# Optimization experiments

Measured on AMD Instinct MI355X. Metric: run time of the kernel, lower is better.

Reference implementation:

```python
import jax, jax.numpy as jnp
import numpy as np

NEG = -1000.0  # fill value for unmatched (type_mask != ti) entries

B, N, R = 4, 48, 16
T = 2 * R + 1          # 33 transition channels
Nc, L = 80, 3          # chains, chain length
Nt, Ni = 16, 5         # triples, chains per triple (uniform c_sections)


def setup_inputs() -> dict:
    key = jax.random.key(0)
    k1, k2, k3, k4, k5 = jax.random.split(key, 5)
    transitions = jax.random.normal(k1, (B, N, N, T), dtype=jnp.float32)
    type_mask = jax.random.randint(k2, (B, N, N, R), 0, 2, dtype=jnp.int32)
    rules = jax.random.randint(k3, (Nc, L), 0, T, dtype=jnp.int32)
    # stacked per-triple weights [Nt, Ni] (orig: ParameterList of [Ni,1]) and biases [Nt]
    weights = jax.random.normal(k4, (Nt, Ni), dtype=jnp.float32) / np.sqrt(Ni)
    biases = jax.random.uniform(k5, (Nt,), dtype=jnp.float32, minval=-1.0, maxval=1.0)
    return {"transitions": transitions, "type_mask": type_mask, "rules": rules,
            "weights": weights, "biases": biases}


def path_scores(transitions, rules):
    """Tropical (max-plus) chain DP.
    transitions: [B,N,N,T], rules: [Nc,L] -> scores [B,N,N,Nc]
    scores[b,x,y,c] = max over intermediate nodes of sum of hop scores.
    """
    Lc = rules.shape[1]
    hops = [transitions[..., rules[:, l]] for l in range(Lc)]  # each [B,N,N,Nc]
    # max-plus "matmul": s[b,x,y,c] = max_k hops0[b,x,k,c] + hops1[b,k,y,c]
    s = jnp.max(hops[0][:, :, :, None, :] + hops[1][:, None, :, :, :], axis=2)
    for l in range(2, Lc):
        s = jnp.max(s[:, :, :, None, :] + hops[l][:, None, :, :, :], axis=2)
    return s


def reference(transitions, type_mask, rules, weights, biases):
    # scores over all chains, exponentiated: [B,N,N,Nc]
    s = jnp.exp(path_scores(transitions, rules))
    # group chains by triple (uniform sections): [B,N,N,Nt,Ni]
    s = s.reshape(s.shape[0], s.shape[1], s.shape[2], Nt, Ni)
    # per-triple weighted sum + bias; one triple per relation so Nt == R
    comb = jnp.einsum('bxytc,tc->bxyt', s, weights) + biases  # [B,N,N,R]
    # masked_scatter: write score where type_mask[...,i] == ti (== 0 here), else -1000
    out = jnp.where(type_mask == 0, comb, NEG)
    return out
```

## Files before the change

kernel.cpp:

```cpp
#include <hip/hip_runtime.h>
#include <cmath>

#define BB 4
#define NN 48
#define PP (NN * NN)
#define TT 33
#define RR 16
#define NC 80
#define NI 5
#define NEG (-1000.0f)

#define XS 24
#define XP 25

__global__ __launch_bounds__(256) void transpose_kernel(
    const float* __restrict__ trans,
    float*       __restrict__ tpose)
{
    __shared__ float tile[64 * TT];
    const int blk = blockIdx.x;
    const int b   = blk / 36;
    const int p0  = (blk - b * 36) * 64;

    const float4* src = (const float4*)(trans + ((size_t)b * PP + p0) * TT);
    for (int j = threadIdx.x; j < 64 * TT / 4; j += 256)
        ((float4*)tile)[j] = src[j];
    __syncthreads();

    for (int j = threadIdx.x; j < TT * 64; j += 256) {
        const int t  = j >> 6;
        const int pl = j & 63;
        tpose[((size_t)b * TT + t) * PP + p0 + pl] = tile[pl * TT + t];
    }
}

__global__ __launch_bounds__(192) void chain_dp_kernel(
    const float* __restrict__ tpose,
    const int*   __restrict__ rules,
    const float* __restrict__ weights,
    float*       __restrict__ sw)
{
    __shared__ float H0T[NN * XP];
    __shared__ float H1 [PP];
    __shared__ float H2 [PP];
    __shared__ float S1T[NN * XP];

    const int blk = blockIdx.x;
    const int bc  = blk >> 1;
    const int xh  = blk & 1;
    const int b   = bc / NC;
    const int c   = bc - b * NC;
    const int xbase = xh * XS;

    const int r0 = rules[c * 3 + 0];
    const int r1 = rules[c * 3 + 1];
    const int r2 = rules[c * 3 + 2];

    const float* p0 = tpose + ((size_t)b * TT + r0) * PP + xbase * NN;
    const float* p1 = tpose + ((size_t)b * TT + r1) * PP;
    const float* p2 = tpose + ((size_t)b * TT + r2) * PP;

    for (int j = threadIdx.x; j < PP / 4; j += 192) {
        ((float4*)H1)[j] = ((const float4*)p1)[j];
        ((float4*)H2)[j] = ((const float4*)p2)[j];
    }
    for (int j = threadIdx.x; j < XS * NN / 4; j += 192) {
        const float4 v0 = ((const float4*)p0)[j];
        const int xl = (4 * j) / NN;
        const int k  = (4 * j) - xl * NN;
        H0T[(k + 0) * XP + xl] = v0.x;
        H0T[(k + 1) * XP + xl] = v0.y;
        H0T[(k + 2) * XP + xl] = v0.z;
        H0T[(k + 3) * XP + xl] = v0.w;
    }
    __syncthreads();

    const int tx = threadIdx.x & 7;
    const int ty = threadIdx.x >> 3;
    const int x0 = tx * 3;
    const int y0 = ty * 2;

    float acc[3][2];
    #pragma unroll
    for (int jx = 0; jx < 3; ++jx) {
        acc[jx][0] = -INFINITY; acc[jx][1] = -INFINITY;
    }

    #pragma unroll 4
    for (int kp = 0; kp < NN / 2; ++kp) {
        const int k = kp * 2;
        float a0[3], a1[3];
        #pragma unroll
        for (int jx = 0; jx < 3; ++jx) {
            a0[jx] = H0T[k * XP + x0 + jx];
            a1[jx] = H0T[(k + 1) * XP + x0 + jx];
        }
        const float2 bv0 = *(const float2*)&H1[k * NN + y0];
        const float2 bv1 = *(const float2*)&H1[(k + 1) * NN + y0];
        #pragma unroll
        for (int jx = 0; jx < 3; ++jx) {
            acc[jx][0] = fmaxf(acc[jx][0], fmaxf(a0[jx] + bv0.x, a1[jx] + bv1.x));
            acc[jx][1] = fmaxf(acc[jx][1], fmaxf(a0[jx] + bv0.y, a1[jx] + bv1.y));
        }
    }

    #pragma unroll
    for (int jx = 0; jx < 3; ++jx) {
        S1T[(y0 + 0) * XP + x0 + jx] = acc[jx][0];
        S1T[(y0 + 1) * XP + x0 + jx] = acc[jx][1];
    }
    __syncthreads();

    float acc2[3][2];
    #pragma unroll
    for (int jx = 0; jx < 3; ++jx) {
        acc2[jx][0] = -INFINITY; acc2[jx][1] = -INFINITY;
    }

    #pragma unroll 4
    for (int kp = 0; kp < NN / 2; ++kp) {
        const int k = kp * 2;
        float a0[3], a1[3];
        #pragma unroll
        for (int jx = 0; jx < 3; ++jx) {
            a0[jx] = S1T[k * XP + x0 + jx];
            a1[jx] = S1T[(k + 1) * XP + x0 + jx];
        }
        const float2 bv0 = *(const float2*)&H2[k * NN + y0];
        const float2 bv1 = *(const float2*)&H2[(k + 1) * NN + y0];
        #pragma unroll
        for (int jx = 0; jx < 3; ++jx) {
            acc2[jx][0] = fmaxf(acc2[jx][0], fmaxf(a0[jx] + bv0.x, a1[jx] + bv1.x));
            acc2[jx][1] = fmaxf(acc2[jx][1], fmaxf(a0[jx] + bv0.y, a1[jx] + bv1.y));
        }
    }

    const float wgt = weights[c];
    float* outp = sw + (size_t)bc * PP;
    #pragma unroll
    for (int jx = 0; jx < 3; ++jx) {
        float2 o;
        o.x = __expf(acc2[jx][0]) * wgt;
        o.y = __expf(acc2[jx][1]) * wgt;
        *(float2*)&outp[(xbase + x0 + jx) * NN + y0] = o;
    }
}

__global__ __launch_bounds__(256) void combine_kernel(
    const float* __restrict__ sw,
    const int*   __restrict__ mask,
    const float* __restrict__ biases,
    float*       __restrict__ out)
{
    const int quad = threadIdx.x >> 6;
    const int pl   = blockIdx.x * 64 + (threadIdx.x & 63);
    const int b = pl / PP;
    const int p = pl - b * PP;

    const float* base = sw + (size_t)b * NC * PP + p;

    float acc[4];
    #pragma unroll
    for (int tt = 0; tt < 4; ++tt) {
        const int t = quad * 4 + tt;
        float s = biases[t];
        #pragma unroll
        for (int i = 0; i < NI; ++i)
            s += base[(size_t)(t * NI + i) * PP];
        acc[tt] = s;
    }

    const int4 m = *(const int4*)(mask + (size_t)pl * RR + quad * 4);
    float4 o;
    o.x = (m.x == 0) ? acc[0] : NEG;
    o.y = (m.y == 0) ? acc[1] : NEG;
    o.z = (m.z == 0) ? acc[2] : NEG;
    o.w = (m.w == 0) ? acc[3] : NEG;
    *(float4*)(out + (size_t)pl * RR + quad * 4) = o;
}

extern "C" void kernel_launch(void* const* d_in, const int* in_sizes, int n_in,
                              void* d_out, int out_size, void* d_ws, size_t ws_size,
                              hipStream_t stream)
{
    const float* trans   = (const float*)d_in[0];
    const int*   mask    = (const int*)  d_in[1];
    const int*   rules   = (const int*)  d_in[2];
    const float* weights = (const float*)d_in[3];
    const float* biases  = (const float*)d_in[4];
    float* out = (float*)d_out;

    float* tpose = (float*)d_ws;
    float* sw    = tpose + (size_t)BB * TT * PP;

    transpose_kernel<<<BB * 36, 256, 0, stream>>>(trans, tpose);

    chain_dp_kernel<<<BB * NC * 2, 192, 0, stream>>>(tpose, rules, weights, sw);

    combine_kernel<<<BB * PP / 64, 256, 0, stream>>>(sw, mask, biases, out);
}
```

Before: 75.38 us.

## Fuse chain DP with per-triple combine and mask, dropping intermediate buffer

The chain DP kernel and the combine kernel are merged. Each block now handles one (batch, triple, x-half), loops over the triple's 5 chains, and accumulates the weighted exp scores in registers before applying bias and mask and writing the output directly. This removes the large intermediate sw buffer round trip and one launch. In exchange the grid shrinks from 640 to 128 blocks, each doing five sequential chain iterations with extra syncs, and the output and mask accesses are strided by 16 and uncoalesced.

```diff
diff --git a/kernel.cpp b/kernel.cpp
--- a/kernel.cpp
+++ b/kernel.cpp
@@ -12,6 +12,7 @@
 
 #define XS 24
 #define XP 25
+#define NTH 384
 
 __global__ __launch_bounds__(256) void transpose_kernel(
     const float* __restrict__ trans,
@@ -34,11 +35,13 @@
     }
 }
 
-__global__ __launch_bounds__(192) void chain_dp_kernel(
+__global__ __launch_bounds__(NTH) void fused_scorer(
     const float* __restrict__ tpose,
     const int*   __restrict__ rules,
     const float* __restrict__ weights,
-    float*       __restrict__ sw)
+    const float* __restrict__ biases,
+    const int*   __restrict__ mask,
+    float*       __restrict__ out)
 {
     __shared__ float H0T[NN * XP];
     __shared__ float H1 [PP];
@@ -46,137 +49,83 @@
     __shared__ float S1T[NN * XP];
 
     const int blk = blockIdx.x;
-    const int bc  = blk >> 1;
     const int xh  = blk & 1;
-    const int b   = bc / NC;
-    const int c   = bc - b * NC;
+    const int bt  = blk >> 1;
+    const int b   = bt >> 4;
+    const int t   = bt & 15;
     const int xbase = xh * XS;
 
-    const int r0 = rules[c * 3 + 0];
-    const int r1 = rules[c * 3 + 1];
-    const int r2 = rules[c * 3 + 2];
+    const int xl = threadIdx.x >> 4;
+    const int yt = threadIdx.x & 15;
+    const int y0 = yt * 3;
 
-    const float* p0 = tpose + ((size_t)b * TT + r0) * PP + xbase * NN;
-    const float* p1 = tpose + ((size_t)b * TT + r1) * PP;
-    const float* p2 = tpose + ((size_t)b * TT + r2) * PP;
+    float acc_out[3] = {0.0f, 0.0f, 0.0f};
 
-    for (int j = threadIdx.x; j < PP / 4; j += 192) {
-        ((float4*)H1)[j] = ((const float4*)p1)[j];
-        ((float4*)H2)[j] = ((const float4*)p2)[j];
-    }
-    for (int j = threadIdx.x; j < XS * NN / 4; j += 192) {
-        const float4 v0 = ((const float4*)p0)[j];
-        const int xl = (4 * j) / NN;
-        const int k  = (4 * j) - xl * NN;
-        H0T[(k + 0) * XP + xl] = v0.x;
-        H0T[(k + 1) * XP + xl] = v0.y;
-        H0T[(k + 2) * XP + xl] = v0.z;
-        H0T[(k + 3) * XP + xl] = v0.w;
-    }
-    __syncthreads();
+    for (int ci = 0; ci < NI; ++ci) {
+        const int c  = t * NI + ci;
+        const int r0 = rules[c * 3 + 0];
+        const int r1 = rules[c * 3 + 1];
+        const int r2 = rules[c * 3 + 2];
+        const float w = weights[c];
 
-    const int tx = threadIdx.x & 7;
-    const int ty = threadIdx.x >> 3;
-    const int x0 = tx * 3;
-    const int y0 = ty * 2;
+        const float* p0 = tpose + ((size_t)b * TT + r0) * PP + xbase * NN;
+        const float* p1 = tpose + ((size_t)b * TT + r1) * PP;
+        const float* p2 = tpose + ((size_t)b * TT + r2) * PP;
 
-    float acc[3][2];
-    #pragma unroll
-    for (int jx = 0; jx < 3; ++jx) {
-        acc[jx][0] = -INFINITY; acc[jx][1] = -INFINITY;
+        __syncthreads();
+
+        for (int j = threadIdx.x; j < PP / 4; j += NTH) {
+            ((float4*)H1)[j] = ((const float4*)p1)[j];
+            ((float4*)H2)[j] = ((const float4*)p2)[j];
+        }
+        for (int j = threadIdx.x; j < XS * NN / 4; j += NTH) {
+            const float4 v0 = ((const float4*)p0)[j];
+            const int x = (4 * j) / NN;
+            const int k = (4 * j) - x * NN;
+            H0T[(k + 0) * XP + x] = v0.x;
+            H0T[(k + 1) * XP + x] = v0.y;
+            H0T[(k + 2) * XP + x] = v0.z;
+            H0T[(k + 3) * XP + x] = v0.w;
+        }
+        __syncthreads();
+
+        float a0 = -INFINITY, a1 = -INFINITY, a2 = -INFINITY;
+        #pragma unroll 4
+        for (int kp = 0; kp < NN / 2; ++kp) {
+            const int k = kp * 2;
+            const float h0 = H0T[k * XP + xl];
+            const float h1 = H0T[(k + 1) * XP + xl];
+            a0 = fmaxf(a0, fmaxf(h0 + H1[k * NN + y0 + 0], h1 + H1[(k + 1) * NN + y0 + 0]));
+            a1 = fmaxf(a1, fmaxf(h0 + H1[k * NN + y0 + 1], h1 + H1[(k + 1) * NN + y0 + 1]));
+            a2 = fmaxf(a2, fmaxf(h0 + H1[k * NN + y0 + 2], h1 + H1[(k + 1) * NN + y0 + 2]));
+        }
+        S1T[(y0 + 0) * XP + xl] = a0;
+        S1T[(y0 + 1) * XP + xl] = a1;
+        S1T[(y0 + 2) * XP + xl] = a2;
+        __syncthreads();
+
+        float s0 = -INFINITY, s1 = -INFINITY, s2 = -INFINITY;
+        #pragma unroll 4
+        for (int kp = 0; kp < NN / 2; ++kp) {
+            const int k = kp * 2;
+            const float h0 = S1T[k * XP + xl];
+            const float h1 = S1T[(k + 1) * XP + xl];
+            s0 = fmaxf(s0, fmaxf(h0 + H2[k * NN + y0 + 0], h1 + H2[(k + 1) * NN + y0 + 0]));
+            s1 = fmaxf(s1, fmaxf(h0 + H2[k * NN + y0 + 1], h1 + H2[(k + 1) * NN + y0 + 1]));
+            s2 = fmaxf(s2, fmaxf(h0 + H2[k * NN + y0 + 2], h1 + H2[(k + 1) * NN + y0 + 2]));
+        }
+        acc_out[0] += w * __expf(s0);
+        acc_out[1] += w * __expf(s1);
+        acc_out[2] += w * __expf(s2);
     }
 
-    #pragma unroll 4
-    for (int kp = 0; kp < NN / 2; ++kp) {
-        const int k = kp * 2;
-        float a0[3], a1[3];
-        #pragma unroll
-        for (int jx = 0; jx < 3; ++jx) {
-            a0[jx] = H0T[k * XP + x0 + jx];
-            a1[jx] = H0T[(k + 1) * XP + x0 + jx];
-        }
-        const float2 bv0 = *(const float2*)&H1[k * NN + y0];
-        const float2 bv1 = *(const float2*)&H1[(k + 1) * NN + y0];
-        #pragma unroll
-        for (int jx = 0; jx < 3; ++jx) {
-            acc[jx][0] = fmaxf(acc[jx][0], fmaxf(a0[jx] + bv0.x, a1[jx] + bv1.x));
-            acc[jx][1] = fmaxf(acc[jx][1], fmaxf(a0[jx] + bv0.y, a1[jx] + bv1.y));
-        }
+    const float bias = biases[t];
+    const int xg = xbase + xl;
+    #pragma unroll
+    for (int j = 0; j < 3; ++j) {
+        const size_t oidx = ((size_t)(b * PP + xg * NN + y0 + j)) * RR + t;
+        out[oidx] = (mask[oidx] == 0) ? (acc_out[j] + bias) : NEG;
     }
-
-    #pragma unroll
-    for (int jx = 0; jx < 3; ++jx) {
-        S1T[(y0 + 0) * XP + x0 + jx] = acc[jx][0];
-        S1T[(y0 + 1) * XP + x0 + jx] = acc[jx][1];
-    }
-    __syncthreads();
-
-    float acc2[3][2];
-    #pragma unroll
-    for (int jx = 0; jx < 3; ++jx) {
-        acc2[jx][0] = -INFINITY; acc2[jx][1] = -INFINITY;
-    }
-
-    #pragma unroll 4
-    for (int kp = 0; kp < NN / 2; ++kp) {
-        const int k = kp * 2;
-        float a0[3], a1[3];
-        #pragma unroll
-        for (int jx = 0; jx < 3; ++jx) {
-            a0[jx] = S1T[k * XP + x0 + jx];
-            a1[jx] = S1T[(k + 1) * XP + x0 + jx];
-        }
-        const float2 bv0 = *(const float2*)&H2[k * NN + y0];
-        const float2 bv1 = *(const float2*)&H2[(k + 1) * NN + y0];
-        #pragma unroll
-        for (int jx = 0; jx < 3; ++jx) {
-            acc2[jx][0] = fmaxf(acc2[jx][0], fmaxf(a0[jx] + bv0.x, a1[jx] + bv1.x));
-            acc2[jx][1] = fmaxf(acc2[jx][1], fmaxf(a0[jx] + bv0.y, a1[jx] + bv1.y));
-        }
-    }
-
-    const float wgt = weights[c];
-    float* outp = sw + (size_t)bc * PP;
-    #pragma unroll
-    for (int jx = 0; jx < 3; ++jx) {
-        float2 o;
-        o.x = __expf(acc2[jx][0]) * wgt;
-        o.y = __expf(acc2[jx][1]) * wgt;
-        *(float2*)&outp[(xbase + x0 + jx) * NN + y0] = o;
-    }
-}
-
-__global__ __launch_bounds__(256) void combine_kernel(
-    const float* __restrict__ sw,
-    const int*   __restrict__ mask,
-    const float* __restrict__ biases,
-    float*       __restrict__ out)
-{
-    const int quad = threadIdx.x >> 6;
-    const int pl   = blockIdx.x * 64 + (threadIdx.x & 63);
-    const int b = pl / PP;
-    const int p = pl - b * PP;
-
-    const float* base = sw + (size_t)b * NC * PP + p;
-
-    float acc[4];
-    #pragma unroll
-    for (int tt = 0; tt < 4; ++tt) {
-        const int t = quad * 4 + tt;
-        float s = biases[t];
-        #pragma unroll
-        for (int i = 0; i < NI; ++i)
-            s += base[(size_t)(t * NI + i) * PP];
-        acc[tt] = s;
-    }
-
-    const int4 m = *(const int4*)(mask + (size_t)pl * RR + quad * 4);
-    float4 o;
-    o.x = (m.x == 0) ? acc[0] : NEG;
-    o.y = (m.y == 0) ? acc[1] : NEG;
-    o.z = (m.z == 0) ? acc[2] : NEG;
-    o.w = (m.w == 0) ? acc[3] : NEG;
-    *(float4*)(out + (size_t)pl * RR + quad * 4) = o;
 }
 
 extern "C" void kernel_launch(void* const* d_in, const int* in_sizes, int n_in,
@@ -191,11 +140,9 @@
     float* out = (float*)d_out;
 
     float* tpose = (float*)d_ws;
-    float* sw    = tpose + (size_t)BB * TT * PP;
 
     transpose_kernel<<<BB * 36, 256, 0, stream>>>(trans, tpose);
 
-    chain_dp_kernel<<<BB * NC * 2, 192, 0, stream>>>(tpose, rules, weights, sw);
-
-    combine_kernel<<<BB * PP / 64, 256, 0, stream>>>(sw, mask, biases, out);
+    fused_scorer<<<BB * RR * 2, NTH, 0, stream>>>(tpose, rules, weights,
+                                                  biases, mask, out);
 }
```

New measurement: 83.02 us. 1.1x slower.
